# Performance work log

Hardware: AMD Instinct MI355X
Metric: run time of the kernel (lower is better)

Reference implementation:

```python
import jax, jax.numpy as jnp
import numpy as np

EMBED_DIM = 1024
NUM_HEADS = 16
HEAD_DIM = EMBED_DIM // NUM_HEADS
B, S = 4, 2048
LN_EPS = 1e-6


def setup_inputs() -> dict:
    key = jax.random.key(0)
    ks = jax.random.split(key, 11)
    sc = 1.0 / np.sqrt(EMBED_DIM)
    inputs = jax.random.normal(ks[0], (B, S, EMBED_DIM), dtype=jnp.float32)
    Wq = jax.random.normal(ks[1], (EMBED_DIM, EMBED_DIM), dtype=jnp.float32) * sc
    bq = jnp.zeros((EMBED_DIM,), jnp.float32)
    Wk = jax.random.normal(ks[2], (EMBED_DIM, EMBED_DIM), dtype=jnp.float32) * sc
    bk = jnp.zeros((EMBED_DIM,), jnp.float32)
    Wv = jax.random.normal(ks[3], (EMBED_DIM, EMBED_DIM), dtype=jnp.float32) * sc
    bv = jnp.zeros((EMBED_DIM,), jnp.float32)
    Wo = jax.random.normal(ks[4], (EMBED_DIM, EMBED_DIM), dtype=jnp.float32) * sc
    bo = jnp.zeros((EMBED_DIM,), jnp.float32)
    gamma = jnp.ones((EMBED_DIM,), jnp.float32)
    beta = jnp.zeros((EMBED_DIM,), jnp.float32)
    return {"inputs": inputs, "Wq": Wq, "bq": bq, "Wk": Wk, "bk": bk,
            "Wv": Wv, "bv": bv, "Wo": Wo, "bo": bo, "gamma": gamma, "beta": beta}


def _attention(inputs, Wq, bq, Wk, bk, Wv, bv, Wo, bo, gamma, beta):
    b, s, d = inputs.shape
    q = (inputs @ Wq + bq).reshape(b, s, NUM_HEADS, HEAD_DIM)
    k = (inputs @ Wk + bk).reshape(b, s, NUM_HEADS, HEAD_DIM)
    v = (inputs @ Wv + bv).reshape(b, s, NUM_HEADS, HEAD_DIM)
    scale = jnp.float32(np.sqrt(HEAD_DIM))
    # [b, h, s, s]
    scores = jnp.einsum('bqhd,bkhd->bhqk', q, k) / scale
    causal = jnp.tril(jnp.ones((s, s), dtype=bool))  # [s, s]
    scores = jnp.where(causal, scores, jnp.float32(-1e9))
    weights = jax.nn.softmax(scores, axis=-1)
    # dropout is identity at inference (training=False)
    attn = jnp.einsum('bhqk,bkhd->bqhd', weights, v).reshape(b, s, d)
    out = attn @ Wo + bo
    resid = inputs + out
    mu = jnp.mean(resid, axis=-1, keepdims=True)
    var = jnp.mean(jnp.square(resid - mu), axis=-1, keepdims=True)
    normed = (resid - mu) / jnp.sqrt(var + LN_EPS) * gamma + beta
    return normed, weights


def reference(inputs, Wq, bq, Wk, bk, Wv, bv, Wo, bo, gamma, beta):
    return _attention(inputs, Wq, bq, Wk, bk, Wv, bv, Wo, bo, gamma, beta)
```

## Files before the change

### kernel.cpp

```cpp
#include <hip/hip_runtime.h>
#include <math.h>

#define B_  4
#define S_  2048
#define D_  1024
#define H_  16
#define DH_ 64
#define M_  (B_*S_)
#define LN_EPS 1e-6f

typedef __attribute__((ext_vector_type(4))) float f32x4;
typedef __attribute__((ext_vector_type(8))) short s16x8;

__device__ __forceinline__ void split2(float x, ushort& h, ushort& l) {
  unsigned u = __float_as_uint(x);
  h = (ushort)(u >> 16);
  float r = x - __uint_as_float(u & 0xFFFF0000u);
  l = (ushort)(__float_as_uint(r) >> 16);
}

__global__ __launch_bounds__(256) void split_kernel(
    const float* __restrict__ in, ushort* __restrict__ hi, ushort* __restrict__ lo)
{
  const size_t t = (size_t)blockIdx.x * 256 + threadIdx.x;
  const float4 a = *(const float4*)(in + t * 8);
  const float4 b = *(const float4*)(in + t * 8 + 4);
  s16x8 hv, lv;
  ushort h, l;
  split2(a.x, h, l); hv[0] = (short)h; lv[0] = (short)l;
  split2(a.y, h, l); hv[1] = (short)h; lv[1] = (short)l;
  split2(a.z, h, l); hv[2] = (short)h; lv[2] = (short)l;
  split2(a.w, h, l); hv[3] = (short)h; lv[3] = (short)l;
  split2(b.x, h, l); hv[4] = (short)h; lv[4] = (short)l;
  split2(b.y, h, l); hv[5] = (short)h; lv[5] = (short)l;
  split2(b.z, h, l); hv[6] = (short)h; lv[6] = (short)l;
  split2(b.w, h, l); hv[7] = (short)h; lv[7] = (short)l;
  *(s16x8*)(hi + t * 8) = hv;
  *(s16x8*)(lo + t * 8) = lv;
}

__global__ __launch_bounds__(256) void splitT_kernel(
    const float* __restrict__ W, ushort* __restrict__ hiT, ushort* __restrict__ loT)
{
  __shared__ float tile[64][65];
  const int n0 = blockIdx.x * 64, k0 = blockIdx.y * 64;
  const int tid = threadIdx.x;
  #pragma unroll
  for (int i = 0; i < 4; ++i) {
    int c = tid + (i << 8);
    int r = c >> 4;
    int c4 = (c & 15) << 2;
    float4 v = *(const float4*)(W + (size_t)(k0 + r) * D_ + n0 + c4);
    tile[r][c4+0] = v.x; tile[r][c4+1] = v.y; tile[r][c4+2] = v.z; tile[r][c4+3] = v.w;
  }
  __syncthreads();
  #pragma unroll
  for (int i = 0; i < 4; ++i) {
    int c = tid + (i << 8);
    int n = c >> 4;
    int k4 = (c & 15) << 2;
    ushort h0,h1,h2,h3, l0,l1,l2,l3;
    split2(tile[k4+0][n], h0, l0);
    split2(tile[k4+1][n], h1, l1);
    split2(tile[k4+2][n], h2, l2);
    split2(tile[k4+3][n], h3, l3);
    size_t o = (size_t)(n0 + n) * D_ + k0 + k4;
    *(ushort4*)(hiT + o) = make_ushort4(h0, h1, h2, h3);
    *(ushort4*)(loT + o) = make_ushort4(l0, l1, l2, l3);
  }
}

#define LDK 40

__global__ __launch_bounds__(256) void gemm_mfma_kernel(
    const ushort* __restrict__ Ahi, const ushort* __restrict__ Alo,
    const ushort* __restrict__ BThi, const ushort* __restrict__ BTlo,
    const float* __restrict__ bias, const float* __restrict__ resid,
    float* __restrict__ C, int M, int N, int K)
{
  __shared__ ushort Ah[128][LDK];
  __shared__ ushort Al[128][LDK];
  __shared__ ushort Bh[128][LDK];
  __shared__ ushort Bl[128][LDK];
  const int tid  = threadIdx.x;
  const int lane = tid & 63;
  const int wid  = tid >> 6;
  const int wm   = wid >> 1, wn = wid & 1;
  const int bm = blockIdx.y * 128, bn = blockIdx.x * 128;

  const int c0 = tid,       r0 = c0 >> 2, k80 = (c0 & 3) << 3;
  const int c1 = tid + 256, r1 = c1 >> 2, k81 = (c1 & 3) << 3;

  f32x4 acc[4][4] = {};

  const int kf = (lane >> 4) << 3;
  const int fm = wm * 64 + (lane & 15);
  const int fn = wn * 64 + (lane & 15);

  for (int k0 = 0; k0 < K; k0 += 32) {
    const size_t ga0 = (size_t)(bm + r0) * K + k0 + k80;
    const size_t ga1 = (size_t)(bm + r1) * K + k0 + k81;
    const size_t gb0 = (size_t)(bn + r0) * K + k0 + k80;
    const size_t gb1 = (size_t)(bn + r1) * K + k0 + k81;
    s16x8 va0 = *(const s16x8*)(Ahi  + ga0);
    s16x8 va1 = *(const s16x8*)(Ahi  + ga1);
    s16x8 ua0 = *(const s16x8*)(Alo  + ga0);
    s16x8 ua1 = *(const s16x8*)(Alo  + ga1);
    s16x8 vb0 = *(const s16x8*)(BThi + gb0);
    s16x8 vb1 = *(const s16x8*)(BThi + gb1);
    s16x8 ub0 = *(const s16x8*)(BTlo + gb0);
    s16x8 ub1 = *(const s16x8*)(BTlo + gb1);
    *(s16x8*)&Ah[r0][k80] = va0;  *(s16x8*)&Ah[r1][k81] = va1;
    *(s16x8*)&Al[r0][k80] = ua0;  *(s16x8*)&Al[r1][k81] = ua1;
    *(s16x8*)&Bh[r0][k80] = vb0;  *(s16x8*)&Bh[r1][k81] = vb1;
    *(s16x8*)&Bl[r0][k80] = ub0;  *(s16x8*)&Bl[r1][k81] = ub1;
    __syncthreads();
    s16x8 ah[4], al[4], bh[4], bl[4];
    #pragma unroll
    for (int i = 0; i < 4; ++i) {
      ah[i] = *(const s16x8*)&Ah[fm + i*16][kf];
      al[i] = *(const s16x8*)&Al[fm + i*16][kf];
      bh[i] = *(const s16x8*)&Bh[fn + i*16][kf];
      bl[i] = *(const s16x8*)&Bl[fn + i*16][kf];
    }
    #pragma unroll
    for (int mi = 0; mi < 4; ++mi) {
      #pragma unroll
      for (int ni = 0; ni < 4; ++ni) {
        acc[mi][ni] = __builtin_amdgcn_mfma_f32_16x16x32_bf16(ah[mi], bh[ni], acc[mi][ni], 0, 0, 0);
        acc[mi][ni] = __builtin_amdgcn_mfma_f32_16x16x32_bf16(al[mi], bh[ni], acc[mi][ni], 0, 0, 0);
        acc[mi][ni] = __builtin_amdgcn_mfma_f32_16x16x32_bf16(ah[mi], bl[ni], acc[mi][ni], 0, 0, 0);
      }
    }
    __syncthreads();
  }
  const int rbase = bm + wm*64 + ((lane >> 4) << 2);
  #pragma unroll
  for (int ni = 0; ni < 4; ++ni) {
    const int col = bn + wn*64 + ni*16 + (lane & 15);
    const float bb = bias[col];
    #pragma unroll
    for (int mi = 0; mi < 4; ++mi) {
      #pragma unroll
      for (int j = 0; j < 4; ++j) {
        const int row = rbase + mi*16 + j;
        float v = acc[mi][ni][j] + bb;
        if (resid) v += resid[(size_t)row * N + col];
        C[(size_t)row * N + col] = v;
      }
    }
  }
}

__device__ __forceinline__ float block_allreduce(float v, bool is_max, float* sbuf) {
  #pragma unroll
  for (int o = 32; o > 0; o >>= 1) {
    float other = __shfl_down(v, o, 64);
    v = is_max ? fmaxf(v, other) : (v + other);
  }
  __syncthreads();
  if ((threadIdx.x & 63) == 0) sbuf[threadIdx.x >> 6] = v;
  __syncthreads();
  float r = sbuf[0];
  #pragma unroll
  for (int w = 1; w < 4; ++w) r = is_max ? fmaxf(r, sbuf[w]) : (r + sbuf[w]);
  return r;
}

#define SQP 72

__global__ __launch_bounds__(256) void scores_mfma_kernel(
    const float* __restrict__ Q, const float* __restrict__ Km,
    float* __restrict__ Wout)
{
  const int kt = blockIdx.x;
  const int qt = blockIdx.y;
  if (kt > 2*qt + 1) return;
  const int bh = blockIdx.z;
  const int b = bh >> 4, h = bh & 15;
  const int q0 = qt * 128, k0 = kt * 64;
  __shared__ ushort Qh[128][SQP], Ql[128][SQP];
  __shared__ ushort Kh[64][SQP],  Kl[64][SQP];
  const int tid = threadIdx.x;
  const int lane = tid & 63, wid = tid >> 6;
  const int wm = wid >> 1, wn = wid & 1;
  const float* Qbase = Q  + ((size_t)b * S_ + q0) * D_ + h * DH_;
  const float* Kbase = Km + ((size_t)b * S_ + k0) * D_ + h * DH_;
  #pragma unroll
  for (int i = 0; i < 8; ++i) {
    int idx = tid + (i << 8);
    int r = idx >> 4, c4 = (idx & 15) << 2;
    float4 v = *(const float4*)(Qbase + (size_t)r * D_ + c4);
    ushort h0,h1,h2,h3,l0,l1,l2,l3;
    split2(v.x,h0,l0); split2(v.y,h1,l1); split2(v.z,h2,l2); split2(v.w,h3,l3);
    *(ushort4*)&Qh[r][c4] = make_ushort4(h0,h1,h2,h3);
    *(ushort4*)&Ql[r][c4] = make_ushort4(l0,l1,l2,l3);
  }
  #pragma unroll
  for (int i = 0; i < 4; ++i) {
    int idx = tid + (i << 8);
    int r = idx >> 4, c4 = (idx & 15) << 2;
    float4 v = *(const float4*)(Kbase + (size_t)r * D_ + c4);
    ushort h0,h1,h2,h3,l0,l1,l2,l3;
    split2(v.x,h0,l0); split2(v.y,h1,l1); split2(v.z,h2,l2); split2(v.w,h3,l3);
    *(ushort4*)&Kh[r][c4] = make_ushort4(h0,h1,h2,h3);
    *(ushort4*)&Kl[r][c4] = make_ushort4(l0,l1,l2,l3);
  }
  __syncthreads();
  const int kf = (lane >> 4) << 3;
  const int fm = wm * 64 + (lane & 15);
  const int fn = wn * 32 + (lane & 15);
  f32x4 acc[4][2] = {};
  #pragma unroll
  for (int d0 = 0; d0 < 64; d0 += 32) {
    s16x8 qa[4], qb[4], ka[2], kb[2];
    #pragma unroll
    for (int mi = 0; mi < 4; ++mi) {
      qa[mi] = *(const s16x8*)&Qh[fm + mi*16][d0 + kf];
      qb[mi] = *(const s16x8*)&Ql[fm + mi*16][d0 + kf];
    }
    #pragma unroll
    for (int ni = 0; ni < 2; ++ni) {
      ka[ni] = *(const s16x8*)&Kh[fn + ni*16][d0 + kf];
      kb[ni] = *(const s16x8*)&Kl[fn + ni*16][d0 + kf];
    }
    #pragma unroll
    for (int mi = 0; mi < 4; ++mi) {
      #pragma unroll
      for (int ni = 0; ni < 2; ++ni) {
        acc[mi][ni] = __builtin_amdgcn_mfma_f32_16x16x32_bf16(qa[mi], ka[ni], acc[mi][ni], 0, 0, 0);
        acc[mi][ni] = __builtin_amdgcn_mfma_f32_16x16x32_bf16(qb[mi], ka[ni], acc[mi][ni], 0, 0, 0);
        acc[mi][ni] = __builtin_amdgcn_mfma_f32_16x16x32_bf16(qa[mi], kb[ni], acc[mi][ni], 0, 0, 0);
      }
    }
  }
  const float scale = 0.125f;
  float* Wrow = Wout + ((size_t)bh * S_ + q0) * S_ + k0;
  const int rb = wm*64 + ((lane >> 4) << 2);
  if ((kt >> 1) < qt) {
    #pragma unroll
    for (int ni = 0; ni < 2; ++ni) {
      const int col = wn*32 + ni*16 + (lane & 15);
      #pragma unroll
      for (int mi = 0; mi < 4; ++mi) {
        #pragma unroll
        for (int j = 0; j < 4; ++j)
          Wrow[(size_t)(rb + mi*16 + j) * S_ + col] = acc[mi][ni][j] * scale;
      }
    }
  } else {
    #pragma unroll
    for (int ni = 0; ni < 2; ++ni) {
      const int col = wn*32 + ni*16 + (lane & 15);
      const int kg = k0 + col;
      #pragma unroll
      for (int mi = 0; mi < 4; ++mi) {
        #pragma unroll
        for (int j = 0; j < 4; ++j) {
          const int row = rb + mi*16 + j;
          if (kg <= q0 + row)
            Wrow[(size_t)row * S_ + col] = acc[mi][ni][j] * scale;
        }
      }
    }
  }
}

__global__ __launch_bounds__(256) void softmax_kernel(float* __restrict__ Wbuf) {
  const int q = blockIdx.x;
  float* row = Wbuf + ((size_t)blockIdx.y * S_ + q) * S_;
  const int valid = q + 1;
  __shared__ float sbuf[4];
  float v[8];
  float lmax = -INFINITY;
  #pragma unroll
  for (int i = 0; i < 8; ++i) {
    int k = threadIdx.x + (i << 8);
    v[i] = (k < valid) ? row[k] : -INFINITY;
    lmax = fmaxf(lmax, v[i]);
  }
  float m = block_allreduce(lmax, true, sbuf);
  float lsum = 0.f;
  #pragma unroll
  for (int i = 0; i < 8; ++i) {
    int k = threadIdx.x + (i << 8);
    v[i] = (k < valid) ? __expf(v[i] - m) : 0.f;
    lsum += v[i];
  }
  float s = block_allreduce(lsum, false, sbuf);
  float inv = 1.f / s;
  #pragma unroll
  for (int i = 0; i < 8; ++i) {
    int k = threadIdx.x + (i << 8);
    row[k] = v[i] * inv;
  }
}

#define PVW 72
#define PVV 74

__global__ __launch_bounds__(256) void pv_mfma_kernel(
    const float* __restrict__ Wbuf, const float* __restrict__ V,
    float* __restrict__ Attn)
{
  const int qt = blockIdx.x, h = blockIdx.y, b = blockIdx.z;
  const int q0 = qt * 128;
  __shared__ ushort Wh[128][PVW], Wl[128][PVW];
  __shared__ ushort Vh[64][PVV],  Vl[64][PVV];
  const int tid = threadIdx.x;
  const int lane = tid & 63, wid = tid >> 6;
  const int wm = wid >> 1, wn = wid & 1;
  f32x4 acc[4][2] = {};
  const size_t wbase = (((size_t)b * H_ + h) * S_ + q0) * S_;
  const float* Vbase = V + (size_t)b * S_ * D_ + h * DH_;
  const int kf = (lane >> 4) << 3;
  const int fm = wm * 64 + (lane & 15);
  const int fn = wn * 32 + (lane & 15);
  const int nkt = 2*qt + 2;
  for (int kt = 0; kt < nkt; ++kt) {
    const int k0 = kt * 64;
    #pragma unroll
    for (int i = 0; i < 8; ++i) {
      int idx = tid + (i << 8);
      int r = idx >> 4, c4 = (idx & 15) << 2;
      float4 v = *(const float4*)(Wbuf + wbase + (size_t)r * S_ + k0 + c4);
      ushort h0,h1,h2,h3,l0,l1,l2,l3;
      split2(v.x,h0,l0); split2(v.y,h1,l1); split2(v.z,h2,l2); split2(v.w,h3,l3);
      *(ushort4*)&Wh[r][c4] = make_ushort4(h0,h1,h2,h3);
      *(ushort4*)&Wl[r][c4] = make_ushort4(l0,l1,l2,l3);
    }
    #pragma unroll
    for (int i = 0; i < 4; ++i) {
      int idx = tid + (i << 8);
      int r = idx >> 4, c4 = (idx & 15) << 2;
      float4 v = *(const float4*)(Vbase + (size_t)(k0 + r) * D_ + c4);
      ushort h0,h1,h2,h3,l0,l1,l2,l3;
      split2(v.x,h0,l0); split2(v.y,h1,l1); split2(v.z,h2,l2); split2(v.w,h3,l3);
      Vh[c4+0][r] = h0; Vh[c4+1][r] = h1; Vh[c4+2][r] = h2; Vh[c4+3][r] = h3;
      Vl[c4+0][r] = l0; Vl[c4+1][r] = l1; Vl[c4+2][r] = l2; Vl[c4+3][r] = l3;
    }
    __syncthreads();
    #pragma unroll
    for (int kk = 0; kk < 64; kk += 32) {
      s16x8 wa[4], wb[4], va[2], vb[2];
      #pragma unroll
      for (int mi = 0; mi < 4; ++mi) {
        wa[mi] = *(const s16x8*)&Wh[fm + mi*16][kk + kf];
        wb[mi] = *(const s16x8*)&Wl[fm + mi*16][kk + kf];
      }
      #pragma unroll
      for (int ni = 0; ni < 2; ++ni) {
        va[ni] = *(const s16x8*)&Vh[fn + ni*16][kk + kf];
        vb[ni] = *(const s16x8*)&Vl[fn + ni*16][kk + kf];
      }
      #pragma unroll
      for (int mi = 0; mi < 4; ++mi) {
        #pragma unroll
        for (int ni = 0; ni < 2; ++ni) {
          acc[mi][ni] = __builtin_amdgcn_mfma_f32_16x16x32_bf16(wa[mi], va[ni], acc[mi][ni], 0, 0, 0);
          acc[mi][ni] = __builtin_amdgcn_mfma_f32_16x16x32_bf16(wb[mi], va[ni], acc[mi][ni], 0, 0, 0);
          acc[mi][ni] = __builtin_amdgcn_mfma_f32_16x16x32_bf16(wa[mi], vb[ni], acc[mi][ni], 0, 0, 0);
        }
      }
    }
    __syncthreads();
  }
  const int rb = q0 + wm*64 + ((lane >> 4) << 2);
  #pragma unroll
  for (int ni = 0; ni < 2; ++ni) {
    const int col = h * DH_ + wn*32 + ni*16 + (lane & 15);
    #pragma unroll
    for (int mi = 0; mi < 4; ++mi) {
      #pragma unroll
      for (int j = 0; j < 4; ++j)
        Attn[((size_t)b * S_ + rb + mi*16 + j) * D_ + col] = acc[mi][ni][j];
    }
  }
}

__global__ __launch_bounds__(256) void ln_kernel(
    const float* __restrict__ R, const float* __restrict__ gamma,
    const float* __restrict__ beta, float* __restrict__ Out)
{
  const int row = blockIdx.x;
  const float* x = R + (size_t)row * D_;
  __shared__ float sbuf[4];
  float4 xv = *(const float4*)(x + threadIdx.x * 4);
  float s  = xv.x + xv.y + xv.z + xv.w;
  float ss = xv.x*xv.x + xv.y*xv.y + xv.z*xv.z + xv.w*xv.w;
  float tot  = block_allreduce(s,  false, sbuf);
  float tot2 = block_allreduce(ss, false, sbuf);
  float mu  = tot  * (1.f / D_);
  float var = tot2 * (1.f / D_) - mu * mu;
  float inv = rsqrtf(var + LN_EPS);
  float4 g  = *(const float4*)(gamma + threadIdx.x * 4);
  float4 be = *(const float4*)(beta  + threadIdx.x * 4);
  float4 o;
  o.x = (xv.x - mu) * inv * g.x + be.x;
  o.y = (xv.y - mu) * inv * g.y + be.y;
  o.z = (xv.z - mu) * inv * g.z + be.z;
  o.w = (xv.w - mu) * inv * g.w + be.w;
  *(float4*)(Out + (size_t)row * D_ + threadIdx.x * 4) = o;
}

extern "C" void kernel_launch(void* const* d_in, const int* in_sizes, int n_in,
                              void* d_out, int out_size, void* d_ws, size_t ws_size,
                              hipStream_t stream) {
  const float* X     = (const float*)d_in[0];
  const float* Wq    = (const float*)d_in[1];
  const float* bq    = (const float*)d_in[2];
  const float* Wk    = (const float*)d_in[3];
  const float* bk    = (const float*)d_in[4];
  const float* Wv    = (const float*)d_in[5];
  const float* bv    = (const float*)d_in[6];
  const float* Wo    = (const float*)d_in[7];
  const float* bo    = (const float*)d_in[8];
  const float* gamma = (const float*)d_in[9];
  const float* beta  = (const float*)d_in[10];

  float* out     = (float*)d_out;
  float* normed  = out;
  float* weights = out + (size_t)B_ * S_ * D_;

  const size_t sz = (size_t)B_ * S_ * D_;
  const size_t wsz = (size_t)D_ * D_;
  float* ws   = (float*)d_ws;
  float* Qb   = ws;
  float* Kb   = ws + sz;
  float* Vb   = ws + 2 * sz;
  float* Attn  = Qb;
  float* Resid = Kb;

  ushort* Xhi  = (ushort*)weights;
  ushort* Xlo  = Xhi + sz;
  ushort* WqHi = Xlo + sz;      ushort* WqLo = WqHi + wsz;
  ushort* WkHi = WqLo + wsz;    ushort* WkLo = WkHi + wsz;
  ushort* WvHi = WkLo + wsz;    ushort* WvLo = WvHi + wsz;
  ushort* AtHi = (ushort*)Vb;   ushort* AtLo = AtHi + sz;
  ushort* WoHi = (ushort*)Qb;   ushort* WoLo = WoHi + wsz;

  dim3 blk(256);
  dim3 gg(D_ / 128, M_ / 128);
  dim3 sg(sz / 2048);

  split_kernel <<<sg, blk, 0, stream>>>(X, Xhi, Xlo);
  splitT_kernel<<<dim3(16,16), blk, 0, stream>>>(Wq, WqHi, WqLo);
  splitT_kernel<<<dim3(16,16), blk, 0, stream>>>(Wk, WkHi, WkLo);
  splitT_kernel<<<dim3(16,16), blk, 0, stream>>>(Wv, WvHi, WvLo);

  gemm_mfma_kernel<<<gg, blk, 0, stream>>>(Xhi, Xlo, WqHi, WqLo, bq, nullptr, Qb, M_, D_, D_);
  gemm_mfma_kernel<<<gg, blk, 0, stream>>>(Xhi, Xlo, WkHi, WkLo, bk, nullptr, Kb, M_, D_, D_);
  gemm_mfma_kernel<<<gg, blk, 0, stream>>>(Xhi, Xlo, WvHi, WvLo, bv, nullptr, Vb, M_, D_, D_);

  scores_mfma_kernel<<<dim3(S_/64, S_/128, B_*H_), blk, 0, stream>>>(Qb, Kb, weights);
  softmax_kernel<<<dim3(S_, B_*H_), blk, 0, stream>>>(weights);
  pv_mfma_kernel<<<dim3(S_/128, H_, B_), blk, 0, stream>>>(weights, Vb, Attn);

  split_kernel <<<sg, blk, 0, stream>>>(Attn, AtHi, AtLo);
  splitT_kernel<<<dim3(16,16), blk, 0, stream>>>(Wo, WoHi, WoLo);
  gemm_mfma_kernel<<<gg, blk, 0, stream>>>(AtHi, AtLo, WoHi, WoLo, bo, X, Resid, M_, D_, D_);

  ln_kernel<<<dim3(M_), blk, 0, stream>>>(Resid, gamma, beta, normed);
}
```

Baseline: 2.122 ms.

## Use direct global-to-LDS loads and emit bf16 hi/lo splits from producer kernels

The GEMM, scores and PV kernels now fill shared memory with global_load_lds 16-byte direct loads into unpadded tiles, where before they went through registers. The QKV projections write bf16 hi/lo halves straight from the epilogue, so scores no longer re-split fp32 Q/K. V gets a separate transpose kernel so PV can load it contiguously with direct loads. PV writes split attention output, which removes the separate split pass before the output projection. The unpadded 32-wide LDS tiles may cause bank conflicts on the MFMA fragment reads, and the workspace buffers are reassigned.

```diff
diff --git a/kernel.cpp b/kernel.cpp
--- a/kernel.cpp
+++ b/kernel.cpp
@@ -11,6 +11,12 @@
 
 typedef __attribute__((ext_vector_type(4))) float f32x4;
 typedef __attribute__((ext_vector_type(8))) short s16x8;
+
+__device__ __forceinline__ void gl16(const void* g, void* l) {
+  __builtin_amdgcn_global_load_lds(
+      (const __attribute__((address_space(1))) unsigned int*)g,
+      (__attribute__((address_space(3))) unsigned int*)l, 16, 0, 0);
+}
 
 __device__ __forceinline__ void split2(float x, ushort& h, ushort& l) {
   unsigned u = __float_as_uint(x);
@@ -70,50 +76,80 @@
   }
 }
 
-#define LDK 40
+__global__ __launch_bounds__(256) void vtrans_kernel(
+    const ushort* __restrict__ Vhi, const ushort* __restrict__ Vlo,
+    ushort* __restrict__ Vthi, ushort* __restrict__ Vtlo)
+{
+  __shared__ ushort Th[64][72], Tl[64][72];
+  const int st = blockIdx.x, h = blockIdx.y, b = blockIdx.z;
+  const int s0 = st * 64;
+  const int tid = threadIdx.x;
+  const ushort* sh = Vhi + ((size_t)(b*S_ + s0)) * D_ + h * DH_;
+  const ushort* sl = Vlo + ((size_t)(b*S_ + s0)) * D_ + h * DH_;
+  #pragma unroll
+  for (int i = 0; i < 4; ++i) {
+    int idx = tid + (i << 8);
+    int r = idx >> 4, c4 = (idx & 15) << 2;
+    *(ushort4*)&Th[r][c4] = *(const ushort4*)(sh + (size_t)r * D_ + c4);
+    *(ushort4*)&Tl[r][c4] = *(const ushort4*)(sl + (size_t)r * D_ + c4);
+  }
+  __syncthreads();
+  ushort* dh = Vthi + ((size_t)(b*H_ + h)) * DH_ * S_ + s0;
+  ushort* dl = Vtlo + ((size_t)(b*H_ + h)) * DH_ * S_ + s0;
+  #pragma unroll
+  for (int i = 0; i < 4; ++i) {
+    int idx = tid + (i << 8);
+    int d = idx >> 4, s4 = (idx & 15) << 2;
+    ushort4 oh = make_ushort4(Th[s4+0][d], Th[s4+1][d], Th[s4+2][d], Th[s4+3][d]);
+    ushort4 ol = make_ushort4(Tl[s4+0][d], Tl[s4+1][d], Tl[s4+2][d], Tl[s4+3][d]);
+    *(ushort4*)(dh + (size_t)d * S_ + s4) = oh;
+    *(ushort4*)(dl + (size_t)d * S_ + s4) = ol;
+  }
+}
 
 __global__ __launch_bounds__(256) void gemm_mfma_kernel(
     const ushort* __restrict__ Ahi, const ushort* __restrict__ Alo,
     const ushort* __restrict__ BThi, const ushort* __restrict__ BTlo,
     const float* __restrict__ bias, const float* __restrict__ resid,
-    float* __restrict__ C, int M, int N, int K)
-{
-  __shared__ ushort Ah[128][LDK];
-  __shared__ ushort Al[128][LDK];
-  __shared__ ushort Bh[128][LDK];
-  __shared__ ushort Bl[128][LDK];
+    float* __restrict__ C, ushort* __restrict__ Chi, ushort* __restrict__ Clo,
+    int M, int N, int K)
+{
+  __shared__ ushort Ah[128][32], Al[128][32], Bh[128][32], Bl[128][32];
   const int tid  = threadIdx.x;
   const int lane = tid & 63;
   const int wid  = tid >> 6;
   const int wm   = wid >> 1, wn = wid & 1;
   const int bm = blockIdx.y * 128, bn = blockIdx.x * 128;
 
-  const int c0 = tid,       r0 = c0 >> 2, k80 = (c0 & 3) << 3;
-  const int c1 = tid + 256, r1 = c1 >> 2, k81 = (c1 & 3) << 3;
+  const int j0 = wid * 128 + lane, j1 = j0 + 64;
+  const int r0 = j0 >> 2, kc0 = (j0 & 3) << 3;
+  const int r1 = j1 >> 2, kc1 = (j1 & 3) << 3;
+  const unsigned off0 = (unsigned)(wid * 128) * 16;
+  const unsigned off1 = off0 + 1024;
+
+  const ushort* a0 = Ahi  + (size_t)(bm + r0) * K + kc0;
+  const ushort* a1 = Ahi  + (size_t)(bm + r1) * K + kc1;
+  const ushort* c0 = Alo  + (size_t)(bm + r0) * K + kc0;
+  const ushort* c1 = Alo  + (size_t)(bm + r1) * K + kc1;
+  const ushort* b0 = BThi + (size_t)(bn + r0) * K + kc0;
+  const ushort* b1 = BThi + (size_t)(bn + r1) * K + kc1;
+  const ushort* d0p = BTlo + (size_t)(bn + r0) * K + kc0;
+  const ushort* d1p = BTlo + (size_t)(bn + r1) * K + kc1;
 
   f32x4 acc[4][4] = {};
-
   const int kf = (lane >> 4) << 3;
   const int fm = wm * 64 + (lane & 15);
   const int fn = wn * 64 + (lane & 15);
 
   for (int k0 = 0; k0 < K; k0 += 32) {
-    const size_t ga0 = (size_t)(bm + r0) * K + k0 + k80;
-    const size_t ga1 = (size_t)(bm + r1) * K + k0 + k81;
-    const size_t gb0 = (size_t)(bn + r0) * K + k0 + k80;
-    const size_t gb1 = (size_t)(bn + r1) * K + k0 + k81;
-    s16x8 va0 = *(const s16x8*)(Ahi  + ga0);
-    s16x8 va1 = *(const s16x8*)(Ahi  + ga1);
-    s16x8 ua0 = *(const s16x8*)(Alo  + ga0);
-    s16x8 ua1 = *(const s16x8*)(Alo  + ga1);
-    s16x8 vb0 = *(const s16x8*)(BThi + gb0);
-    s16x8 vb1 = *(const s16x8*)(BThi + gb1);
-    s16x8 ub0 = *(const s16x8*)(BTlo + gb0);
-    s16x8 ub1 = *(const s16x8*)(BTlo + gb1);
-    *(s16x8*)&Ah[r0][k80] = va0;  *(s16x8*)&Ah[r1][k81] = va1;
-    *(s16x8*)&Al[r0][k80] = ua0;  *(s16x8*)&Al[r1][k81] = ua1;
-    *(s16x8*)&Bh[r0][k80] = vb0;  *(s16x8*)&Bh[r1][k81] = vb1;
-    *(s16x8*)&Bl[r0][k80] = ub0;  *(s16x8*)&Bl[r1][k81] = ub1;
+    gl16(a0 + k0, (char*)&Ah[0][0] + off0);
+    gl16(a1 + k0, (char*)&Ah[0][0] + off1);
+    gl16(c0 + k0, (char*)&Al[0][0] + off0);
+    gl16(c1 + k0, (char*)&Al[0][0] + off1);
+    gl16(b0 + k0, (char*)&Bh[0][0] + off0);
+    gl16(b1 + k0, (char*)&Bh[0][0] + off1);
+    gl16(d0p + k0, (char*)&Bl[0][0] + off0);
+    gl16(d1p + k0, (char*)&Bl[0][0] + off1);
     __syncthreads();
     s16x8 ah[4], al[4], bh[4], bl[4];
     #pragma unroll
@@ -145,8 +181,14 @@
       for (int j = 0; j < 4; ++j) {
         const int row = rbase + mi*16 + j;
         float v = acc[mi][ni][j] + bb;
-        if (resid) v += resid[(size_t)row * N + col];
-        C[(size_t)row * N + col] = v;
+        const size_t off = (size_t)row * N + col;
+        if (Chi) {
+          ushort h, l; split2(v, h, l);
+          Chi[off] = h; Clo[off] = l;
+        } else {
+          if (resid) v += resid[off];
+          C[off] = v;
+        }
       }
     }
   }
@@ -167,10 +209,9 @@
   return r;
 }
 
-#define SQP 72
-
 __global__ __launch_bounds__(256) void scores_mfma_kernel(
-    const float* __restrict__ Q, const float* __restrict__ Km,
+    const ushort* __restrict__ Qhi, const ushort* __restrict__ Qlo,
+    const ushort* __restrict__ Khi, const ushort* __restrict__ Klo,
     float* __restrict__ Wout)
 {
   const int kt = blockIdx.x;
@@ -179,32 +220,32 @@
   const int bh = blockIdx.z;
   const int b = bh >> 4, h = bh & 15;
   const int q0 = qt * 128, k0 = kt * 64;
-  __shared__ ushort Qh[128][SQP], Ql[128][SQP];
-  __shared__ ushort Kh[64][SQP],  Kl[64][SQP];
+  __shared__ ushort Qh2[2][128][32], Ql2[2][128][32];
+  __shared__ ushort Kh2[2][64][32],  Kl2[2][64][32];
   const int tid = threadIdx.x;
   const int lane = tid & 63, wid = tid >> 6;
   const int wm = wid >> 1, wn = wid & 1;
-  const float* Qbase = Q  + ((size_t)b * S_ + q0) * D_ + h * DH_;
-  const float* Kbase = Km + ((size_t)b * S_ + k0) * D_ + h * DH_;
-  #pragma unroll
-  for (int i = 0; i < 8; ++i) {
-    int idx = tid + (i << 8);
-    int r = idx >> 4, c4 = (idx & 15) << 2;
-    float4 v = *(const float4*)(Qbase + (size_t)r * D_ + c4);
-    ushort h0,h1,h2,h3,l0,l1,l2,l3;
-    split2(v.x,h0,l0); split2(v.y,h1,l1); split2(v.z,h2,l2); split2(v.w,h3,l3);
-    *(ushort4*)&Qh[r][c4] = make_ushort4(h0,h1,h2,h3);
-    *(ushort4*)&Ql[r][c4] = make_ushort4(l0,l1,l2,l3);
-  }
+  const ushort* qh = Qhi + ((size_t)(b*S_ + q0)) * D_ + h * DH_;
+  const ushort* ql = Qlo + ((size_t)(b*S_ + q0)) * D_ + h * DH_;
+  const ushort* kh = Khi + ((size_t)(b*S_ + k0)) * D_ + h * DH_;
+  const ushort* kl = Klo + ((size_t)(b*S_ + k0)) * D_ + h * DH_;
   #pragma unroll
   for (int i = 0; i < 4; ++i) {
-    int idx = tid + (i << 8);
-    int r = idx >> 4, c4 = (idx & 15) << 2;
-    float4 v = *(const float4*)(Kbase + (size_t)r * D_ + c4);
-    ushort h0,h1,h2,h3,l0,l1,l2,l3;
-    split2(v.x,h0,l0); split2(v.y,h1,l1); split2(v.z,h2,l2); split2(v.w,h3,l3);
-    *(ushort4*)&Kh[r][c4] = make_ushort4(h0,h1,h2,h3);
-    *(ushort4*)&Kl[r][c4] = make_ushort4(l0,l1,l2,l3);
+    int jj = wid * 256 + i * 64 + lane;
+    int row = (jj >> 2) & 127;
+    int d = ((jj >> 9) << 5) + ((jj & 3) << 3);
+    unsigned lb = (unsigned)(wid * 256 + i * 64 - lane) * 16 + (unsigned)lane * 16;
+    gl16(qh + (size_t)row * D_ + d, (char*)&Qh2[0][0][0] + (unsigned)(jj - lane) * 16);
+    gl16(ql + (size_t)row * D_ + d, (char*)&Ql2[0][0][0] + (unsigned)(jj - lane) * 16);
+    (void)lb;
+  }
+  #pragma unroll
+  for (int i = 0; i < 2; ++i) {
+    int jj = wid * 128 + i * 64 + lane;
+    int row = (jj >> 2) & 63;
+    int d = ((jj >> 8) << 5) + ((jj & 3) << 3);
+    gl16(kh + (size_t)row * D_ + d, (char*)&Kh2[0][0][0] + (unsigned)(jj - lane) * 16);
+    gl16(kl + (size_t)row * D_ + d, (char*)&Kl2[0][0][0] + (unsigned)(jj - lane) * 16);
   }
   __syncthreads();
   const int kf = (lane >> 4) << 3;
@@ -212,17 +253,17 @@
   const int fn = wn * 32 + (lane & 15);
   f32x4 acc[4][2] = {};
   #pragma unroll
-  for (int d0 = 0; d0 < 64; d0 += 32) {
+  for (int hd = 0; hd < 2; ++hd) {
     s16x8 qa[4], qb[4], ka[2], kb[2];
     #pragma unroll
     for (int mi = 0; mi < 4; ++mi) {
-      qa[mi] = *(const s16x8*)&Qh[fm + mi*16][d0 + kf];
-      qb[mi] = *(const s16x8*)&Ql[fm + mi*16][d0 + kf];
+      qa[mi] = *(const s16x8*)&Qh2[hd][fm + mi*16][kf];
+      qb[mi] = *(const s16x8*)&Ql2[hd][fm + mi*16][kf];
     }
     #pragma unroll
     for (int ni = 0; ni < 2; ++ni) {
-      ka[ni] = *(const s16x8*)&Kh[fn + ni*16][d0 + kf];
-      kb[ni] = *(const s16x8*)&Kl[fn + ni*16][d0 + kf];
+      ka[ni] = *(const s16x8*)&Kh2[hd][fn + ni*16][kf];
+      kb[ni] = *(const s16x8*)&Kl2[hd][fn + ni*16][kf];
     }
     #pragma unroll
     for (int mi = 0; mi < 4; ++mi) {
@@ -296,23 +337,22 @@
   }
 }
 
-#define PVW 72
-#define PVV 74
-
 __global__ __launch_bounds__(256) void pv_mfma_kernel(
-    const float* __restrict__ Wbuf, const float* __restrict__ V,
-    float* __restrict__ Attn)
+    const float* __restrict__ Wbuf,
+    const ushort* __restrict__ Vthi, const ushort* __restrict__ Vtlo,
+    ushort* __restrict__ AtHi, ushort* __restrict__ AtLo)
 {
   const int qt = blockIdx.x, h = blockIdx.y, b = blockIdx.z;
   const int q0 = qt * 128;
-  __shared__ ushort Wh[128][PVW], Wl[128][PVW];
-  __shared__ ushort Vh[64][PVV],  Vl[64][PVV];
+  __shared__ ushort Wh2[2][128][32], Wl2[2][128][32];
+  __shared__ ushort Vh2[2][64][32],  Vl2[2][64][32];
   const int tid = threadIdx.x;
   const int lane = tid & 63, wid = tid >> 6;
   const int wm = wid >> 1, wn = wid & 1;
   f32x4 acc[4][2] = {};
   const size_t wbase = (((size_t)b * H_ + h) * S_ + q0) * S_;
-  const float* Vbase = V + (size_t)b * S_ * D_ + h * DH_;
+  const ushort* vth = Vthi + ((size_t)(b*H_ + h)) * DH_ * S_;
+  const ushort* vtl = Vtlo + ((size_t)(b*H_ + h)) * DH_ * S_;
   const int kf = (lane >> 4) << 3;
   const int fm = wm * 64 + (lane & 15);
   const int fn = wn * 32 + (lane & 15);
@@ -320,38 +360,37 @@
   for (int kt = 0; kt < nkt; ++kt) {
     const int k0 = kt * 64;
     #pragma unroll
+    for (int i = 0; i < 2; ++i) {
+      int jj = wid * 128 + i * 64 + lane;
+      int drow = (jj >> 2) & 63;
+      int kk = ((jj >> 8) << 5) + ((jj & 3) << 3);
+      gl16(vth + (size_t)drow * S_ + k0 + kk, (char*)&Vh2[0][0][0] + (unsigned)(jj - lane) * 16);
+      gl16(vtl + (size_t)drow * S_ + k0 + kk, (char*)&Vl2[0][0][0] + (unsigned)(jj - lane) * 16);
+    }
+    #pragma unroll
     for (int i = 0; i < 8; ++i) {
       int idx = tid + (i << 8);
       int r = idx >> 4, c4 = (idx & 15) << 2;
       float4 v = *(const float4*)(Wbuf + wbase + (size_t)r * S_ + k0 + c4);
       ushort h0,h1,h2,h3,l0,l1,l2,l3;
       split2(v.x,h0,l0); split2(v.y,h1,l1); split2(v.z,h2,l2); split2(v.w,h3,l3);
-      *(ushort4*)&Wh[r][c4] = make_ushort4(h0,h1,h2,h3);
-      *(ushort4*)&Wl[r][c4] = make_ushort4(l0,l1,l2,l3);
-    }
-    #pragma unroll
-    for (int i = 0; i < 4; ++i) {
-      int idx = tid + (i << 8);
-      int r = idx >> 4, c4 = (idx & 15) << 2;
-      float4 v = *(const float4*)(Vbase + (size_t)(k0 + r) * D_ + c4);
-      ushort h0,h1,h2,h3,l0,l1,l2,l3;
-      split2(v.x,h0,l0); split2(v.y,h1,l1); split2(v.z,h2,l2); split2(v.w,h3,l3);
-      Vh[c4+0][r] = h0; Vh[c4+1][r] = h1; Vh[c4+2][r] = h2; Vh[c4+3][r] = h3;
-      Vl[c4+0][r] = l0; Vl[c4+1][r] = l1; Vl[c4+2][r] = l2; Vl[c4+3][r] = l3;
+      int hf = c4 >> 5, cl = c4 & 31;
+      *(ushort4*)&Wh2[hf][r][cl] = make_ushort4(h0,h1,h2,h3);
+      *(ushort4*)&Wl2[hf][r][cl] = make_ushort4(l0,l1,l2,l3);
     }
     __syncthreads();
     #pragma unroll
-    for (int kk = 0; kk < 64; kk += 32) {
+    for (int hf = 0; hf < 2; ++hf) {
       s16x8 wa[4], wb[4], va[2], vb[2];
       #pragma unroll
       for (int mi = 0; mi < 4; ++mi) {
-        wa[mi] = *(const s16x8*)&Wh[fm + mi*16][kk + kf];
-        wb[mi] = *(const s16x8*)&Wl[fm + mi*16][kk + kf];
+        wa[mi] = *(const s16x8*)&Wh2[hf][fm + mi*16][kf];
+        wb[mi] = *(const s16x8*)&Wl2[hf][fm + mi*16][kf];
       }
       #pragma unroll
       for (int ni = 0; ni < 2; ++ni) {
-        va[ni] = *(const s16x8*)&Vh[fn + ni*16][kk + kf];
-        vb[ni] = *(const s16x8*)&Vl[fn + ni*16][kk + kf];
+        va[ni] = *(const s16x8*)&Vh2[hf][fn + ni*16][kf];
+        vb[ni] = *(const s16x8*)&Vl2[hf][fn + ni*16][kf];
       }
       #pragma unroll
       for (int mi = 0; mi < 4; ++mi) {
@@ -372,8 +411,11 @@
     #pragma unroll
     for (int mi = 0; mi < 4; ++mi) {
       #pragma unroll
-      for (int j = 0; j < 4; ++j)
-        Attn[((size_t)b * S_ + rb + mi*16 + j) * D_ + col] = acc[mi][ni][j];
+      for (int j = 0; j < 4; ++j) {
+        size_t off = ((size_t)b * S_ + rb + mi*16 + j) * D_ + col;
+        ushort hh, ll; split2(acc[mi][ni][j], hh, ll);
+        AtHi[off] = hh; AtLo[off] = ll;
+      }
     }
   }
 }
@@ -424,20 +466,21 @@
 
   const size_t sz = (size_t)B_ * S_ * D_;
   const size_t wsz = (size_t)D_ * D_;
-  float* ws   = (float*)d_ws;
-  float* Qb   = ws;
-  float* Kb   = ws + sz;
-  float* Vb   = ws + 2 * sz;
-  float* Attn  = Qb;
-  float* Resid = Kb;
-
-  ushort* Xhi  = (ushort*)weights;
-  ushort* Xlo  = Xhi + sz;
-  ushort* WqHi = Xlo + sz;      ushort* WqLo = WqHi + wsz;
-  ushort* WkHi = WqLo + wsz;    ushort* WkLo = WkHi + wsz;
-  ushort* WvHi = WkLo + wsz;    ushort* WvLo = WvHi + wsz;
-  ushort* AtHi = (ushort*)Vb;   ushort* AtLo = AtHi + sz;
-  ushort* WoHi = (ushort*)Qb;   ushort* WoLo = WoHi + wsz;
+
+  ushort* u = (ushort*)d_ws;
+  ushort* Qhi  = u;            ushort* Qlo  = u + sz;
+  ushort* Khi  = u + 2*sz;     ushort* Klo  = u + 3*sz;
+  ushort* Vthi = u + 4*sz;     ushort* Vtlo = u + 5*sz;
+  ushort* AtHi = u;            ushort* AtLo = u + sz;
+  ushort* WoHi = u + 2*sz;     ushort* WoLo = WoHi + wsz;
+  float*  Resid = (float*)(u + 4*sz);
+
+  ushort* w0   = (ushort*)weights;
+  ushort* Xhi  = w0;           ushort* Xlo  = w0 + sz;
+  ushort* WqHi = w0 + 2*sz;            ushort* WqLo = WqHi + wsz;
+  ushort* WkHi = WqLo + wsz;           ushort* WkLo = WkHi + wsz;
+  ushort* WvHi = WkLo + wsz;           ushort* WvLo = WvHi + wsz;
+  ushort* Vhi  = WvLo + wsz;           ushort* Vlo  = Vhi + sz;
 
   dim3 blk(256);
   dim3 gg(D_ / 128, M_ / 128);
@@ -448,17 +491,24 @@
   splitT_kernel<<<dim3(16,16), blk, 0, stream>>>(Wk, WkHi, WkLo);
   splitT_kernel<<<dim3(16,16), blk, 0, stream>>>(Wv, WvHi, WvLo);
 
-  gemm_mfma_kernel<<<gg, blk, 0, stream>>>(Xhi, Xlo, WqHi, WqLo, bq, nullptr, Qb, M_, D_, D_);
-  gemm_mfma_kernel<<<gg, blk, 0, stream>>>(Xhi, Xlo, WkHi, WkLo, bk, nullptr, Kb, M_, D_, D_);
-  gemm_mfma_kernel<<<gg, blk, 0, stream>>>(Xhi, Xlo, WvHi, WvLo, bv, nullptr, Vb, M_, D_, D_);
-
-  scores_mfma_kernel<<<dim3(S_/64, S_/128, B_*H_), blk, 0, stream>>>(Qb, Kb, weights);
+  gemm_mfma_kernel<<<gg, blk, 0, stream>>>(Xhi, Xlo, WqHi, WqLo, bq, nullptr,
+                                           nullptr, Qhi, Qlo, M_, D_, D_);
+  gemm_mfma_kernel<<<gg, blk, 0, stream>>>(Xhi, Xlo, WkHi, WkLo, bk, nullptr,
+                                           nullptr, Khi, Klo, M_, D_, D_);
+  gemm_mfma_kernel<<<gg, blk, 0, stream>>>(Xhi, Xlo, WvHi, WvLo, bv, nullptr,
+                                           nullptr, Vhi, Vlo, M_, D_, D_);
+
+  vtrans_kernel<<<dim3(S_/64, H_, B_), blk, 0, stream>>>(Vhi, Vlo, Vthi, Vtlo);
+
+  scores_mfma_kernel<<<dim3(S_/64, S_/128, B_*H_), blk, 0, stream>>>(
+      Qhi, Qlo, Khi, Klo, weights);
   softmax_kernel<<<dim3(S_, B_*H_), blk, 0, stream>>>(weights);
-  pv_mfma_kernel<<<dim3(S_/128, H_, B_), blk, 0, stream>>>(weights, Vb, Attn);
-
-  split_kernel <<<sg, blk, 0, stream>>>(Attn, AtHi, AtLo);
+  pv_mfma_kernel<<<dim3(S_/128, H_, B_), blk, 0, stream>>>(
+      weights, Vthi, Vtlo, AtHi, AtLo);
+
   splitT_kernel<<<dim3(16,16), blk, 0, stream>>>(Wo, WoHi, WoLo);
-  gemm_mfma_kernel<<<gg, blk, 0, stream>>>(AtHi, AtLo, WoHi, WoLo, bo, X, Resid, M_, D_, D_);
+  gemm_mfma_kernel<<<gg, blk, 0, stream>>>(AtHi, AtLo, WoHi, WoLo, bo, X,
+                                           Resid, nullptr, nullptr, M_, D_, D_);
 
   ln_kernel<<<dim3(M_), blk, 0, stream>>>(Resid, gamma, beta, normed);
 }
```

Measured after the change: 2.252 ms. 6.1% more time.
